# Performance work log

Hardware: AMD Instinct MI355X
Metric: run time of the kernel (lower is better)

Reference implementation:

```python
import jax, jax.numpy as jnp
import numpy as np

NEG_INF = -1000000000.0
NEG_SLOPE = 0.01  # torch leaky_relu default

N, IN_F, OUT_F = 8192, 256, 128


def setup_inputs() -> dict:
    key = jax.random.key(0)
    k1, k2, k3, k4 = jax.random.split(key, 4)
    x = jax.random.normal(k1, (N, IN_F), dtype=jnp.float32)
    adj = jax.random.randint(k2, (N, N), 0, 2, dtype=jnp.int32)
    W = jax.random.normal(k3, (IN_F, OUT_F), dtype=jnp.float32) * (1.0 / np.sqrt(IN_F))
    a = jax.random.normal(k4, (2 * OUT_F,), dtype=jnp.float32) * (1.0 / np.sqrt(2 * OUT_F))
    return {"x": x, "adj": adj, "W": W, "a": a}


def reference(x, adj, W, a):
    # h = W(x): [N, out]
    h = x @ W
    out_f = h.shape[1]
    # a([h_i || h_j]) == h_i @ a1 + h_j @ a2 -- same math, no [N,N,2F] tensor
    a1, a2 = a[:out_f], a[out_f:]
    f1 = h @ a1  # [N]
    f2 = h @ a2  # [N]
    e = jax.nn.leaky_relu(f1[:, None] + f2[None, :], negative_slope=NEG_SLOPE)  # [N, N]
    masked = jnp.where(adj > 0, e, NEG_INF)
    attention = jax.nn.softmax(masked, axis=1)
    return attention @ h, attention
```

## Files before the change

kernel.cpp:

```cpp
#include <hip/hip_runtime.h>
#include <hip/hip_bf16.h>

constexpr int NROW = 8192;
constexpr int INF  = 256;
constexpr int OUTF = 128;
constexpr int KSPLIT = 8;
constexpr int KCHUNK = NROW / KSPLIT;
constexpr int NIT    = KCHUNK / 64;
#define LOG2E 1.4426950408889634f

typedef __bf16 bf16x8 __attribute__((ext_vector_type(8)));
typedef float  f32x4  __attribute__((ext_vector_type(4)));
typedef int    i32x4  __attribute__((ext_vector_type(4)));
typedef unsigned long long u64;

#define GLOAD_LDS16(gsrc, ldst)                                           \
  __builtin_amdgcn_global_load_lds(                                       \
      (const __attribute__((address_space(1))) unsigned int*)(gsrc),      \
      (__attribute__((address_space(3))) unsigned int*)(ldst), 16, 0, 0)

__global__ __launch_bounds__(256) void k1(const float* __restrict__ x,
                                          const float* __restrict__ W,
                                          const float* __restrict__ a,
                                          __bf16* __restrict__ ht,
                                          float* __restrict__ f1,
                                          float* __restrict__ f2) {
  __shared__ float xs[32][INF];
  __shared__ float hs[32][OUTF];
  const int t  = threadIdx.x;
  const int i0 = blockIdx.x * 32;

  const f32x4* xsrc = reinterpret_cast<const f32x4*>(x + (size_t)i0 * INF);
  f32x4* xdst = reinterpret_cast<f32x4*>(&xs[0][0]);
  #pragma unroll
  for (int u = 0; u < (32 * INF / 4) / 256; ++u)
    xdst[u * 256 + t] = xsrc[u * 256 + t];
  __syncthreads();

  const int c  = t & 127;
  const int rg = t >> 7;
  float acc[16];
  #pragma unroll
  for (int r = 0; r < 16; ++r) acc[r] = 0.f;
  for (int k = 0; k < INF; ++k) {
    float wv = W[k * OUTF + c];
    #pragma unroll
    for (int r = 0; r < 16; ++r) acc[r] += xs[rg * 16 + r][k] * wv;
  }
  #pragma unroll
  for (int r = 0; r < 16; ++r) hs[rg * 16 + r][c] = acc[r];
  __syncthreads();

  const int wv = t >> 6, lane = t & 63;
  for (int r = wv; r < 32; r += 4) {
    float h0 = hs[r][lane * 2], h1 = hs[r][lane * 2 + 1];
    float s1 = h0 * a[lane * 2] + h1 * a[lane * 2 + 1];
    float s2 = h0 * a[OUTF + lane * 2] + h1 * a[OUTF + lane * 2 + 1];
    #pragma unroll
    for (int off = 32; off; off >>= 1) {
      s1 += __shfl_down(s1, off);
      s2 += __shfl_down(s2, off);
    }
    if (lane == 0) { f1[i0 + r] = s1 * LOG2E; f2[i0 + r] = s2 * LOG2E; }
  }

  const int col = t >> 1, seg = t & 1;
  bf16x8 v0, v1;
  #pragma unroll
  for (int r = 0; r < 8; ++r) v0[r] = (__bf16)hs[seg * 16 + r][col];
  #pragma unroll
  for (int r = 0; r < 8; ++r) v1[r] = (__bf16)hs[seg * 16 + 8 + r][col];
  __bf16* hdst = ht + (size_t)col * NROW + i0 + seg * 16;
  *reinterpret_cast<bf16x8*>(hdst)     = v0;
  *reinterpret_cast<bf16x8*>(hdst + 8) = v1;
}

__global__ __launch_bounds__(256) void k2(const int* __restrict__ adj,
                                          const float* __restrict__ f1,
                                          const float* __restrict__ f2,
                                          u64* __restrict__ mask,
                                          float* __restrict__ s) {
  const int row  = blockIdx.x * 4 + (threadIdx.x >> 6);
  const int lane = threadIdx.x & 63;
  const float f1i = f1[row];
  const i32x4* arow = reinterpret_cast<const i32x4*>(adj + (size_t)row * NROW);
  const f32x4* f2v  = reinterpret_cast<const f32x4*>(f2);

  float acc = 0.f;
  for (int it = 0; it < NROW / 512; ++it) {
    i32x4 av0 = __builtin_nontemporal_load(arow + it * 128 + lane);
    i32x4 av1 = __builtin_nontemporal_load(arow + it * 128 + 64 + lane);
    f32x4 fv0 = f2v[it * 128 + lane];
    f32x4 fv1 = f2v[it * 128 + 64 + lane];

    unsigned nib0 = (av0[0] > 0) | ((av0[1] > 0) << 1) | ((av0[2] > 0) << 2) |
                    ((av0[3] > 0) << 3);
    unsigned nib1 = (av1[0] > 0) | ((av1[1] > 0) << 1) | ((av1[2] > 0) << 2) |
                    ((av1[3] > 0) << 3);
    #pragma unroll
    for (int b = 0; b < 4; ++b) {
      float e0 = f1i + fv0[b];
      e0 = e0 > 0.f ? e0 : 0.01f * e0;
      acc += ((nib0 >> b) & 1u) ? __builtin_exp2f(e0) : 0.f;
      float e1 = f1i + fv1[b];
      e1 = e1 > 0.f ? e1 : 0.01f * e1;
      acc += ((nib1 >> b) & 1u) ? __builtin_exp2f(e1) : 0.f;
    }
    u64 m0 = (u64)nib0 << (4 * (lane & 15));
    u64 m1 = (u64)nib1 << (4 * (lane & 15));
    #pragma unroll
    for (int d = 1; d < 16; d <<= 1) {
      m0 |= __shfl_xor(m0, d);
      m1 |= __shfl_xor(m1, d);
    }
    if ((lane & 15) == 0) {
      mask[(size_t)row * 128 + it * 8 + (lane >> 4)]     = m0;
      mask[(size_t)row * 128 + it * 8 + 4 + (lane >> 4)] = m1;
    }
  }
  #pragma unroll
  for (int off = 32; off; off >>= 1) acc += __shfl_down(acc, off);
  if (lane == 0) s[row] = acc;
}

__global__ __launch_bounds__(256, 3) void k3f(const __bf16* __restrict__ ht,
                                              const float* __restrict__ f1,
                                              const float* __restrict__ f2,
                                              const float* __restrict__ sum,
                                              const u64* __restrict__ mask,
                                              float* __restrict__ out0,
                                              float* __restrict__ att) {
  __shared__ alignas(16) char smem[45568];
  const int bid = blockIdx.x;
  const int q  = bid / 9;
  const int r9 = bid % 9;
  const int t  = threadIdx.x;

  if (r9 != 0) {
    const int row = q * 8 + (r9 - 1);
    u64* msl = reinterpret_cast<u64*>(smem);
    if (t < 128) msl[t] = mask[(size_t)row * 128 + t];
    const float f1i   = f1[row];
    const float inv_s = 1.0f / sum[row];
    const f32x4* f2v  = reinterpret_cast<const f32x4*>(f2);
    f32x4 fv[8];
    #pragma unroll
    for (int it = 0; it < 8; ++it) fv[it] = f2v[it * 256 + t];
    __syncthreads();
    unsigned mynibs = 0;
    #pragma unroll
    for (int it = 0; it < 8; ++it)
      mynibs |= ((unsigned)(msl[it * 16 + (t >> 4)] >> ((t & 15) * 4)) & 0xFu)
                << (it * 4);
    f32x4* adst = reinterpret_cast<f32x4*>(att + (size_t)row * NROW);
    #pragma unroll
    for (int it = 0; it < 8; ++it) {
      const unsigned nib = (mynibs >> (it * 4)) & 0xFu;
      f32x4 o;
      #pragma unroll
      for (int b = 0; b < 4; ++b) {
        float e = f1i + fv[it][b];
        e = e > 0.f ? e : 0.01f * e;
        o[b] = ((nib >> b) & 1u) ? __builtin_exp2f(e) * inv_s : 0.f;
      }
      adst[it * 256 + t] = o;
    }
    return;
  }

  __bf16 (*bs)[128 * 64] = reinterpret_cast<__bf16(*)[128 * 64]>(smem);
  float* f2s = reinterpret_cast<float*>(smem + 32768);
  u64 (*ms)[17] = reinterpret_cast<u64(*)[17]>(smem + 32768 + 4096);

  const int mb = q / KSPLIT;
  const int ks = q % KSPLIT;
  const int w    = t >> 6;
  const int lane = t & 63;
  const int lr = lane & 15;
  const int lc = lane >> 4;
  const int row0 = mb * 64;
  const int j0 = ks * KCHUNK;

  const int srow = w * 32 + (lane >> 3);
  const int sgcol = ((lane & 7) ^ ((lane >> 3) & 7)) << 3;
  const __bf16* sgbase = ht + (size_t)srow * NROW + j0 + sgcol;
  const int ldsu = w * 2048;

  reinterpret_cast<f32x4*>(f2s)[t] =
      reinterpret_cast<const f32x4*>(f2 + j0)[t];
  {
    const int rr = t >> 2, qq = (t & 3) * 4;
    const u64* msrc = mask + (size_t)(row0 + rr) * 128 + (j0 >> 6) + qq;
    ms[rr][qq]     = msrc[0];
    ms[rr][qq + 1] = msrc[1];
    ms[rr][qq + 2] = msrc[2];
    ms[rr][qq + 3] = msrc[3];
  }
  #pragma unroll
  for (int qq = 0; qq < 4; ++qq)
    GLOAD_LDS16(sgbase + (size_t)(qq * 8) * NROW, &bs[0][ldsu + qq * 512]);
  __syncthreads();

  const int   rloc = w * 16 + lr;
  const float f1r  = f1[row0 + rloc];
  const int   s0 = (lc ^ (lr & 7)) << 3;
  const int   s1 = ((lc + 4) ^ (lr & 7)) << 3;

  f32x4 acc[8];
  #pragma unroll
  for (int n = 0; n < 8; ++n) acc[n] = (f32x4){0.f, 0.f, 0.f, 0.f};

  for (int it = 0; it < NIT; ++it) {
    const int cur = it & 1;
    const bool more = (it + 1) < NIT;
    const int kk = it * 64;

    if (more) {
      #pragma unroll
      for (int qq = 0; qq < 4; ++qq)
        GLOAD_LDS16(sgbase + (size_t)(qq * 8) * NROW + kk + 64,
                    &bs[cur ^ 1][ldsu + qq * 512]);
    }

    const u64 mw = ms[rloc][it];
    bf16x8 afrag[2];
    #pragma unroll
    for (int h = 0; h < 2; ++h) {
      const unsigned bits = (unsigned)(mw >> (h * 32 + lc * 8)) & 0xFFu;
      const int base = kk + h * 32 + lc * 8;
      #pragma unroll
      for (int i2 = 0; i2 < 8; ++i2) {
        float e = f1r + f2s[base + i2];
        e = e > 0.f ? e : 0.01f * e;
        afrag[h][i2] = (__bf16)(((bits >> i2) & 1u) ? __builtin_exp2f(e) : 0.f);
      }
    }

    #pragma unroll
    for (int n = 0; n < 8; ++n) {
      const int rb = (n * 16 + lr) * 64;
      bf16x8 b0 = *reinterpret_cast<const bf16x8*>(&bs[cur][rb + s0]);
      bf16x8 b1 = *reinterpret_cast<const bf16x8*>(&bs[cur][rb + s1]);
      acc[n] = __builtin_amdgcn_mfma_f32_16x16x32_bf16(afrag[0], b0, acc[n], 0, 0, 0);
      acc[n] = __builtin_amdgcn_mfma_f32_16x16x32_bf16(afrag[1], b1, acc[n], 0, 0, 0);
    }

    if (more) __syncthreads();
  }

  float inv_sD[4];
  #pragma unroll
  for (int i2 = 0; i2 < 4; ++i2)
    inv_sD[i2] = 1.0f / sum[row0 + w * 16 + lc * 4 + i2];
  #pragma unroll
  for (int n = 0; n < 8; ++n) {
    #pragma unroll
    for (int i2 = 0; i2 < 4; ++i2) {
      atomicAdd(&out0[(size_t)(row0 + w * 16 + lc * 4 + i2) * OUTF + n * 16 + lr],
                acc[n][i2] * inv_sD[i2]);
    }
  }
}

extern "C" void kernel_launch(void* const* d_in, const int* in_sizes, int n_in,
                              void* d_out, int out_size, void* d_ws, size_t ws_size,
                              hipStream_t stream) {
  const float* x   = (const float*)d_in[0];
  const int*   adj = (const int*)d_in[1];
  const float* W   = (const float*)d_in[2];
  const float* a   = (const float*)d_in[3];

  float* out0 = (float*)d_out;
  float* att  = (float*)d_out + (size_t)NROW * OUTF;

  char* ws = (char*)d_ws;
  __bf16* ht = (__bf16*)ws;
  u64* mask = (u64*)(ws + (2 << 20));
  float* f1 = (float*)(ws + (10 << 20));
  float* f2 = (float*)(ws + (10 << 20) + 32 * 1024);
  float* s  = (float*)(ws + (10 << 20) + 64 * 1024);

  hipMemsetAsync(out0, 0, (size_t)NROW * OUTF * sizeof(float), stream);
  k1<<<NROW / 32, 256, 0, stream>>>(x, W, a, ht, f1, f2);
  k2<<<NROW / 4, 256, 0, stream>>>(adj, f1, f2, mask, s);
  k3f<<<9216, 256, 0, stream>>>(ht, f1, f2, s, mask, out0, att);
}
```

Before: 181.1 us.

## Single-buffer k3f LDS for higher occupancy, fold output zeroing into k1

Result: faster. 164.5 us, median of 2 (-9.2%).

```diff
diff --git a/kernel.cpp b/kernel.cpp
--- a/kernel.cpp
+++ b/kernel.cpp
@@ -24,35 +24,43 @@
                                           const float* __restrict__ a,
                                           __bf16* __restrict__ ht,
                                           float* __restrict__ f1,
-                                          float* __restrict__ f2) {
-  __shared__ float xs[32][INF];
-  __shared__ float hs[32][OUTF];
+                                          float* __restrict__ f2,
+                                          float* __restrict__ out0) {
+  __shared__ float xs[16][INF];
+  __shared__ float hs[16][OUTF];
   const int t  = threadIdx.x;
-  const int i0 = blockIdx.x * 32;
+  const int i0 = blockIdx.x * 16;
+
+  {
+    f32x4 z = (f32x4){0.f, 0.f, 0.f, 0.f};
+    f32x4* od = reinterpret_cast<f32x4*>(out0 + (size_t)i0 * OUTF);
+    od[t]       = z;
+    od[t + 256] = z;
+  }
 
   const f32x4* xsrc = reinterpret_cast<const f32x4*>(x + (size_t)i0 * INF);
   f32x4* xdst = reinterpret_cast<f32x4*>(&xs[0][0]);
   #pragma unroll
-  for (int u = 0; u < (32 * INF / 4) / 256; ++u)
+  for (int u = 0; u < (16 * INF / 4) / 256; ++u)
     xdst[u * 256 + t] = xsrc[u * 256 + t];
   __syncthreads();
 
   const int c  = t & 127;
   const int rg = t >> 7;
-  float acc[16];
-  #pragma unroll
-  for (int r = 0; r < 16; ++r) acc[r] = 0.f;
+  float acc[8];
+  #pragma unroll
+  for (int r = 0; r < 8; ++r) acc[r] = 0.f;
   for (int k = 0; k < INF; ++k) {
     float wv = W[k * OUTF + c];
     #pragma unroll
-    for (int r = 0; r < 16; ++r) acc[r] += xs[rg * 16 + r][k] * wv;
-  }
-  #pragma unroll
-  for (int r = 0; r < 16; ++r) hs[rg * 16 + r][c] = acc[r];
+    for (int r = 0; r < 8; ++r) acc[r] += xs[rg * 8 + r][k] * wv;
+  }
+  #pragma unroll
+  for (int r = 0; r < 8; ++r) hs[rg * 8 + r][c] = acc[r];
   __syncthreads();
 
   const int wv = t >> 6, lane = t & 63;
-  for (int r = wv; r < 32; r += 4) {
+  for (int r = wv; r < 16; r += 4) {
     float h0 = hs[r][lane * 2], h1 = hs[r][lane * 2 + 1];
     float s1 = h0 * a[lane * 2] + h1 * a[lane * 2 + 1];
     float s2 = h0 * a[OUTF + lane * 2] + h1 * a[OUTF + lane * 2 + 1];
@@ -65,14 +73,10 @@
   }
 
   const int col = t >> 1, seg = t & 1;
-  bf16x8 v0, v1;
-  #pragma unroll
-  for (int r = 0; r < 8; ++r) v0[r] = (__bf16)hs[seg * 16 + r][col];
-  #pragma unroll
-  for (int r = 0; r < 8; ++r) v1[r] = (__bf16)hs[seg * 16 + 8 + r][col];
-  __bf16* hdst = ht + (size_t)col * NROW + i0 + seg * 16;
-  *reinterpret_cast<bf16x8*>(hdst)     = v0;
-  *reinterpret_cast<bf16x8*>(hdst + 8) = v1;
+  bf16x8 v0;
+  #pragma unroll
+  for (int r = 0; r < 8; ++r) v0[r] = (__bf16)hs[seg * 8 + r][col];
+  *reinterpret_cast<bf16x8*>(ht + (size_t)col * NROW + i0 + seg * 8) = v0;
 }
 
 __global__ __launch_bounds__(256) void k2(const int* __restrict__ adj,
@@ -123,14 +127,14 @@
   if (lane == 0) s[row] = acc;
 }
 
-__global__ __launch_bounds__(256, 3) void k3f(const __bf16* __restrict__ ht,
+__global__ __launch_bounds__(256, 5) void k3f(const __bf16* __restrict__ ht,
                                               const float* __restrict__ f1,
                                               const float* __restrict__ f2,
                                               const float* __restrict__ sum,
                                               const u64* __restrict__ mask,
                                               float* __restrict__ out0,
                                               float* __restrict__ att) {
-  __shared__ alignas(16) char smem[45568];
+  __shared__ alignas(16) char smem[29184];
   const int bid = blockIdx.x;
   const int q  = bid / 9;
   const int r9 = bid % 9;
@@ -168,9 +172,9 @@
     return;
   }
 
-  __bf16 (*bs)[128 * 64] = reinterpret_cast<__bf16(*)[128 * 64]>(smem);
-  float* f2s = reinterpret_cast<float*>(smem + 32768);
-  u64 (*ms)[17] = reinterpret_cast<u64(*)[17]>(smem + 32768 + 4096);
+  __bf16* bs = reinterpret_cast<__bf16*>(smem);
+  float* f2s = reinterpret_cast<float*>(smem + 16384);
+  u64 (*ms)[17] = reinterpret_cast<u64(*)[17]>(smem + 20480);
 
   const int mb = q / KSPLIT;
   const int ks = q % KSPLIT;
@@ -196,9 +200,6 @@
     ms[rr][qq + 2] = msrc[2];
     ms[rr][qq + 3] = msrc[3];
   }
-  #pragma unroll
-  for (int qq = 0; qq < 4; ++qq)
-    GLOAD_LDS16(sgbase + (size_t)(qq * 8) * NROW, &bs[0][ldsu + qq * 512]);
   __syncthreads();
 
   const int   rloc = w * 16 + lr;
@@ -211,16 +212,14 @@
   for (int n = 0; n < 8; ++n) acc[n] = (f32x4){0.f, 0.f, 0.f, 0.f};
 
   for (int it = 0; it < NIT; ++it) {
-    const int cur = it & 1;
-    const bool more = (it + 1) < NIT;
     const int kk = it * 64;
 
-    if (more) {
-      #pragma unroll
-      for (int qq = 0; qq < 4; ++qq)
-        GLOAD_LDS16(sgbase + (size_t)(qq * 8) * NROW + kk + 64,
-                    &bs[cur ^ 1][ldsu + qq * 512]);
-    }
+    if (it) __syncthreads();
+
+    #pragma unroll
+    for (int qq = 0; qq < 4; ++qq)
+      GLOAD_LDS16(sgbase + (size_t)(qq * 8) * NROW + kk,
+                  &bs[ldsu + qq * 512]);
 
     const u64 mw = ms[rloc][it];
     bf16x8 afrag[2];
@@ -236,16 +235,16 @@
       }
     }
 
+    __syncthreads();
+
     #pragma unroll
     for (int n = 0; n < 8; ++n) {
       const int rb = (n * 16 + lr) * 64;
-      bf16x8 b0 = *reinterpret_cast<const bf16x8*>(&bs[cur][rb + s0]);
-      bf16x8 b1 = *reinterpret_cast<const bf16x8*>(&bs[cur][rb + s1]);
+      bf16x8 b0 = *reinterpret_cast<const bf16x8*>(&bs[rb + s0]);
+      bf16x8 b1 = *reinterpret_cast<const bf16x8*>(&bs[rb + s1]);
       acc[n] = __builtin_amdgcn_mfma_f32_16x16x32_bf16(afrag[0], b0, acc[n], 0, 0, 0);
       acc[n] = __builtin_amdgcn_mfma_f32_16x16x32_bf16(afrag[1], b1, acc[n], 0, 0, 0);
     }
-
-    if (more) __syncthreads();
   }
 
   float inv_sD[4];
@@ -280,8 +279,7 @@
   float* f2 = (float*)(ws + (10 << 20) + 32 * 1024);
   float* s  = (float*)(ws + (10 << 20) + 64 * 1024);
 
-  hipMemsetAsync(out0, 0, (size_t)NROW * OUTF * sizeof(float), stream);
-  k1<<<NROW / 32, 256, 0, stream>>>(x, W, a, ht, f1, f2);
+  k1<<<NROW / 16, 256, 0, stream>>>(x, W, a, ht, f1, f2, out0);
   k2<<<NROW / 4, 256, 0, stream>>>(adj, f1, f2, mask, s);
   k3f<<<9216, 256, 0, stream>>>(ht, f1, f2, s, mask, out0, att);
 }
```
